# Optimization experiments

Hardware: AMD Instinct MI355X
Metric: run time of the kernel (lower is better)

## Reference

```python
import jax, jax.numpy as jnp
import numpy as np

OBS_DIM = 64; ACT_DIM = 18; INTER = 64; COMMAND = 32
UNITS = ACT_DIM + COMMAND + INTER  # 114; neuron order: [motor, command, inter]
Q_HIDDEN = max(32, UNITS)
B, T = 2048, 64
ODE_UNFOLDS = 6
EPS = 1e-8


def _build_wiring(seed=0):
    """NCP sparse wiring: sensory->inter, inter->command, command recurrent, command->motor."""
    rng = np.random.default_rng(seed)
    adj = np.zeros((UNITS, UNITS), np.float32)   # [pre, post]
    sens = np.zeros((OBS_DIM, UNITS), np.float32)
    motor = np.arange(ACT_DIM)
    cmd = np.arange(ACT_DIM, ACT_DIM + COMMAND)
    inter = np.arange(ACT_DIM + COMMAND, UNITS)
    for s in range(OBS_DIM):
        for d in rng.choice(inter, size=8, replace=False):
            sens[s, d] = rng.choice([-1.0, 1.0])
    for i in inter:
        for d in rng.choice(cmd, size=8, replace=False):
            adj[i, d] = rng.choice([-1.0, 1.0])
    for _ in range(32):
        adj[rng.choice(cmd), rng.choice(cmd)] = rng.choice([-1.0, 1.0])
    for m in motor:
        for s in rng.choice(cmd, size=8, replace=False):
            adj[s, m] = rng.choice([-1.0, 1.0])
    return adj, sens


def setup_inputs() -> dict:
    key = jax.random.key(0)
    ks = jax.random.split(key, 16)
    adj, sens = _build_wiring()
    u = lambda k, shape, lo, hi: jax.random.uniform(k, shape, jnp.float32, lo, hi)
    return {
        "obs": jax.random.normal(ks[0], (B, T, OBS_DIM), jnp.float32),
        "hidden": jnp.zeros((B, UNITS), jnp.float32),
        "input_w": jnp.ones((OBS_DIM,), jnp.float32),
        "input_b": jnp.zeros((OBS_DIM,), jnp.float32),
        "sensory_w": u(ks[1], (OBS_DIM, UNITS), 0.001, 1.0),
        "sensory_mu": u(ks[2], (OBS_DIM, UNITS), 0.3, 0.8),
        "sensory_sigma": u(ks[3], (OBS_DIM, UNITS), 3.0, 8.0),
        "sensory_erev": jnp.asarray(sens),
        "sensory_mask": jnp.asarray(np.abs(sens)),
        "w": u(ks[4], (UNITS, UNITS), 0.001, 1.0),
        "mu": u(ks[5], (UNITS, UNITS), 0.3, 0.8),
        "sigma": u(ks[6], (UNITS, UNITS), 3.0, 8.0),
        "erev": jnp.asarray(adj),
        "mask": jnp.asarray(np.abs(adj)),
        "gleak": u(ks[7], (UNITS,), 0.001, 1.0),
        "vleak": u(ks[8], (UNITS,), -0.2, 0.2),
        "cm": u(ks[9], (UNITS,), 0.4, 0.6),
        "q_w1": jax.random.normal(ks[10], (UNITS, Q_HIDDEN), jnp.float32) / np.sqrt(UNITS).astype(np.float32),
        "q_b1": jnp.zeros((Q_HIDDEN,), jnp.float32),
        "q_w2": jax.random.normal(ks[11], (Q_HIDDEN, ACT_DIM), jnp.float32) / np.sqrt(Q_HIDDEN).astype(np.float32),
        "q_b2": jnp.zeros((ACT_DIM,), jnp.float32),
    }


def _ltc_forward(obs, hidden, input_w, input_b, sensory_w, sensory_mu, sensory_sigma,
                 sensory_erev, sensory_mask, w, mu, sigma, erev, mask, gleak, vleak, cm):
    sw = sensory_w * sensory_mask          # sparse sensory synapses (S, U)
    ww = w * mask                          # sparse recurrent synapses (U, U)
    cm_t = cm * ODE_UNFOLDS                # cm / (elapsed_time / ode_unfolds), elapsed_time = 1.0

    @jax.checkpoint
    def step(h, x):
        xi = x * input_w + input_b                                                    # (B, S) affine input map
        s_act = sw * jax.nn.sigmoid((xi[:, :, None] - sensory_mu) * sensory_sigma)    # (B, S, U)
        w_num_s = jnp.sum(s_act * sensory_erev, axis=1)                               # (B, U)
        w_den_s = jnp.sum(s_act, axis=1)                                              # (B, U)

        def unfold(v, _):
            act = ww * jax.nn.sigmoid((v[:, :, None] - mu) * sigma)                   # (B, U, U)
            num = cm_t * v + gleak * vleak + jnp.sum(act * erev, axis=1) + w_num_s
            den = cm_t + gleak + jnp.sum(act, axis=1) + w_den_s
            return num / (den + EPS), None

        v, _ = jax.lax.scan(unfold, h, None, length=ODE_UNFOLDS)
        return v, None

    h, _ = jax.lax.scan(step, hidden, jnp.swapaxes(obs, 0, 1))  # scan over time
    return h


def reference(obs, hidden, input_w, input_b, sensory_w, sensory_mu, sensory_sigma,
              sensory_erev, sensory_mask, w, mu, sigma, erev, mask, gleak, vleak, cm,
              q_w1, q_b1, q_w2, q_b2):
    h = _ltc_forward(obs, hidden, input_w, input_b, sensory_w, sensory_mu, sensory_sigma,
                     sensory_erev, sensory_mask, w, mu, sigma, erev, mask, gleak, vleak, cm)
    q = jax.nn.relu(h @ q_w1 + q_b1) @ q_w2 + q_b2  # Q-head over full hidden state
    return q, h
```

## Files before the change

kernel.cpp:

```cpp
#include <hip/hip_runtime.h>

#define UNITS   114
#define SDIM    64
#define ACT     18
#define TSTEPS  64

#define CR 13
#define CS 9
#define ER_CAP 704
#define MSTRIDE 24

#define LOG2E 1.4426950408889634f
#define EPS   1e-8f

__device__ __forceinline__ float bperm(int addr, float v) {
  return __int_as_float(__builtin_amdgcn_ds_bpermute(addr, __float_as_int(v)));
}
__device__ __forceinline__ float dperm(int addr, float v) {
  return __int_as_float(__builtin_amdgcn_ds_permute(addr, __float_as_int(v)));
}
__device__ __forceinline__ float sigm(float msl, float nsgl, float x) {
  return __builtin_amdgcn_rcpf(1.f + __builtin_amdgcn_exp2f(fmaf(x, nsgl, msl)));
}
__device__ __forceinline__ void wsync() {
  __builtin_amdgcn_fence(__ATOMIC_ACQ_REL, "wavefront");
  __builtin_amdgcn_wave_barrier();
}
__device__ __forceinline__ int canonLane(int u) { return (u >= 64) ? (u - 64) : u; }

__device__ __forceinline__ int kthSetBit(unsigned long long m, int k) {
  int pos = 0;
#pragma unroll
  for (int ww = 32; ww >= 1; ww >>= 1) {
    const unsigned long long lowMask = ((1ull << ww) - 1ull);
    const int c = __popcll(m & lowMask);
    if (k >= c) { k -= c; m >>= ww; pos += ww; }
  }
  return pos;
}

__global__ __launch_bounds__(64) void build_all(
    const float* __restrict__ w,  const float* __restrict__ mu,
    const float* __restrict__ sigma, const float* __restrict__ erev,
    const float* __restrict__ mask,
    const float* __restrict__ sw, const float* __restrict__ smu,
    const float* __restrict__ ssg, const float* __restrict__ serev,
    const float* __restrict__ smask,
    float4* __restrict__ recP4, float2* __restrict__ recP2, int* __restrict__ recAd,
    float4* __restrict__ senP4, float2* __restrict__ senP2, int* __restrict__ senAd,
    int* __restrict__ meta)
{
  const int l = threadIdx.x;
  __shared__ short ePre[ER_CAP], ePIdx[ER_CAP];
  __shared__ int deg[64], off[65];
  __shared__ int pLane[64], pF0[64], pRole[64];
  __shared__ int contIdx[64], contOwn[64], splitRole[64], split2[64], ownP[128];
  __shared__ int rcv[64];

  contIdx[l] = 0; contOwn[l] = 0; splitRole[l] = -1; split2[l] = 0;
  ownP[2*l] = -1; ownP[2*l+1] = -1;
  pLane[l] = 0; pF0[l] = 0; pRole[l] = 0;

  if (blockIdx.x == 0) {
    int d = 0;
    if (l < 50) for (int i = 18; i < UNITS; ++i) d += (mask[i*UNITS + l] != 0.f) ? 1 : 0;
    deg[l] = (l < 50) ? d : 0;
    __syncthreads();
    if (l == 0) { int a = 0; for (int j = 0; j < 64; ++j) { off[j] = a; a += deg[j]; } off[64] = a; }
    __syncthreads();
    if (l < 50) {
      int o = off[l];
      for (int i = 18; i < UNITS; ++i)
        if (mask[i*UNITS + l] != 0.f) { ePre[o] = (short)i; ePIdx[o] = (short)l; ++o; }
    }
    if (l == 0) {
      int lam = 0, f = 0, pc = 0;
      for (int p = 0; p < 50; ++p) {
        const int dd = deg[p];
        if (pc == 2 || f == CR || dd > 3*CR - f) { ++lam; f = 0; pc = 0; }
        if (lam > 63) lam = 63;
        pLane[p] = lam; pF0[p] = f; pRole[p] = pc;
        ownP[2*lam + pc] = p;
        const int owner = lam, role = pc; ++pc;
        const int take = dd < (CR - f) ? dd : (CR - f);
        f += take; int rem = dd - take;
        if (rem > 0) {
          splitRole[owner] = role; split2[owner] = (rem > CR) ? 1 : 0;
          ++lam; if (lam > 63) lam = 63; contIdx[lam] = 1; contOwn[lam] = owner; pc = 1;
          const int t2 = rem < CR ? rem : CR; f = t2; rem -= t2;
          if (rem > 0) { ++lam; if (lam > 63) lam = 63; contIdx[lam] = 2; contOwn[lam] = owner; pc = 1; f = rem; }
        }
      }
    }
    __syncthreads();
    int dA = (contIdx[l] == 1) ? contOwn[l] : -1;
    int dB = (contIdx[l] == 2) ? contOwn[l] : -1;
    rcv[l] = 0; __syncthreads();
    if (dA >= 0) rcv[dA] = 1;
    __syncthreads();
    {
      const unsigned long long recvM = __ballot(rcv[l] != 0);
      const unsigned long long dumm  = __ballot(dA < 0);
      if (dA < 0) dA = kthSetBit(~recvM, __popcll(dumm & ((1ull << l) - 1ull)));
    }
    __syncthreads();
    rcv[l] = 0; __syncthreads();
    if (dB >= 0) rcv[dB] = 1;
    __syncthreads();
    {
      const unsigned long long recvM = __ballot(rcv[l] != 0);
      const unsigned long long dumm  = __ballot(dB < 0);
      if (dB < 0) dB = kthSetBit(~recvM, __popcll(dumm & ((1ull << l) - 1ull)));
    }
    {
      int* M = meta + l * MSTRIDE;
      M[0] = dA * 4; M[1] = dB * 4;
      const float s1A = (splitRole[l] == 0) ? 1.f : 0.f, s1B = (splitRole[l] == 1) ? 1.f : 0.f;
      M[2] = __float_as_int(s1A); M[3] = __float_as_int(s1B);
      const float s2 = split2[l] ? 1.f : 0.f;
      M[4] = __float_as_int(s1A * s2); M[5] = __float_as_int(s1B * s2);
      const int uA = ownP[2*l], uB = ownP[2*l+1];
      M[6] = ((uA >= 0) ? uA : 128 + l) * 4;
      M[7] = ((uB >= 0) ? uB : 192 + l) * 4;
      M[8] = (uA >= 0) ? uA : 0;
      M[9] = (uB >= 0) ? uB : 0;
    }
    for (int t = l; t < CR*64; t += 64) {
      recP4[t] = make_float4(0.f,0.f,0.f,0.f); recP2[t] = make_float2(0.f,0.f); recAd[t] = 0;
    }
    __syncthreads();
    {
      const int E = off[64];
      for (int e = l; e < E; e += 64) {
        const int pre = ePre[e], pj = ePIdx[e];
        const int r  = e - off[pj];
        const int dd = deg[pj], f0 = pF0[pj], role0 = pRole[pj];
        const int take = dd < (CR - f0) ? dd : (CR - f0);
        int lane = pLane[pj], slot, role;
        if (r < take)            { slot = f0 + r;        role = role0; }
        else if (r < take + CR)  { lane += 1; slot = r - take;      role = 0; }
        else                     { lane += 2; slot = r - take - CR; role = 0; }
        if (lane > 63) lane = 63;
        const int idx = pre * UNITS + pj;
        const float sg = sigma[idx];
        const float nsgl = -sg * LOG2E, msl = mu[idx] * sg * LOG2E;
        const float wd = w[idx], wn = wd * erev[idx];
        const int tt = slot * 64 + lane;
        recP4[tt] = make_float4(nsgl, msl, role ? 0.f : wn, role ? 0.f : wd);
        recP2[tt] = role ? make_float2(wn, wd) : make_float2(0.f, 0.f);
        recAd[tt] = pre * 4;
      }
    }
  } else {
    int d = 0;
    { const int col = 50 + l; for (int i = 0; i < SDIM; ++i) d += (smask[i*UNITS + col] != 0.f) ? 1 : 0; }
    deg[l] = d;
    __syncthreads();
    if (l == 0) { int a = 0; for (int j = 0; j < 64; ++j) { off[j] = a; a += deg[j]; } off[64] = a; }
    __syncthreads();
    {
      int o = off[l]; const int col = 50 + l;
      for (int i = 0; i < SDIM; ++i)
        if (smask[i*UNITS + col] != 0.f) { ePre[o] = (short)i; ePIdx[o] = (short)l; ++o; }
    }
    if (l == 0) {
      int lam = 0, f = 0, pc = 0;
      for (int p = 0; p < 64; ++p) {
        const int dd = deg[p];
        if (pc == 2 || f == CS || dd > 3*CS - f) { ++lam; f = 0; pc = 0; }
        if (lam > 63) lam = 63;
        pLane[p] = lam; pF0[p] = f; pRole[p] = pc;
        ownP[2*lam + pc] = p;
        const int owner = lam, role = pc; ++pc;
        const int take = dd < (CS - f) ? dd : (CS - f);
        f += take; int rem = dd - take;
        if (rem > 0) {
          splitRole[owner] = role; split2[owner] = (rem > CS) ? 1 : 0;
          ++lam; if (lam > 63) lam = 63; contIdx[lam] = 1; contOwn[lam] = owner; pc = 1;
          const int t2 = rem < CS ? rem : CS; f = t2; rem -= t2;
          if (rem > 0) { ++lam; if (lam > 63) lam = 63; contIdx[lam] = 2; contOwn[lam] = owner; pc = 1; f = rem; }
        }
      }
    }
    __syncthreads();
    int dA = (contIdx[l] == 1) ? contOwn[l] : -1;
    int dB = (contIdx[l] == 2) ? contOwn[l] : -1;
    rcv[l] = 0; __syncthreads();
    if (dA >= 0) rcv[dA] = 1;
    __syncthreads();
    {
      const unsigned long long recvM = __ballot(rcv[l] != 0);
      const unsigned long long dumm  = __ballot(dA < 0);
      if (dA < 0) dA = kthSetBit(~recvM, __popcll(dumm & ((1ull << l) - 1ull)));
    }
    __syncthreads();
    rcv[l] = 0; __syncthreads();
    if (dB >= 0) rcv[dB] = 1;
    __syncthreads();
    {
      const unsigned long long recvM = __ballot(rcv[l] != 0);
      const unsigned long long dumm  = __ballot(dB < 0);
      if (dB < 0) dB = kthSetBit(~recvM, __popcll(dumm & ((1ull << l) - 1ull)));
    }
    __syncthreads();
    int rA = (ownP[2*l]   >= 0) ? canonLane(50 + ownP[2*l])   : -1;
    int rB = (ownP[2*l+1] >= 0) ? canonLane(50 + ownP[2*l+1]) : -1;
    rcv[l] = 0; __syncthreads();
    if (rA >= 0) rcv[rA] = 1;
    __syncthreads();
    const int isRcvA = rcv[l];
    {
      const unsigned long long recvM = __ballot(isRcvA != 0);
      const unsigned long long dumm  = __ballot(rA < 0);
      if (rA < 0) rA = kthSetBit(~recvM, __popcll(dumm & ((1ull << l) - 1ull)));
    }
    __syncthreads();
    rcv[l] = 0; __syncthreads();
    if (rB >= 0) rcv[rB] = 1;
    __syncthreads();
    {
      const unsigned long long recvM = __ballot(rcv[l] != 0);
      const unsigned long long dumm  = __ballot(rB < 0);
      if (rB < 0) rB = kthSetBit(~recvM, __popcll(dumm & ((1ull << l) - 1ull)));
    }
    {
      int* M = meta + l * MSTRIDE;
      M[10] = dA * 4; M[11] = dB * 4;
      const float s1A = (splitRole[l] == 0) ? 1.f : 0.f, s1B = (splitRole[l] == 1) ? 1.f : 0.f;
      M[12] = __float_as_int(s1A); M[13] = __float_as_int(s1B);
      const float s2 = split2[l] ? 1.f : 0.f;
      M[14] = __float_as_int(s1A * s2); M[15] = __float_as_int(s1B * s2);
      M[16] = rA * 4; M[17] = rB * 4;
      M[18] = __float_as_int(isRcvA ? 1.f : 0.f);
      M[19] = __float_as_int(isRcvA ? 0.f : 1.f);
      const int pA = ownP[2*l], pB = ownP[2*l+1];
      M[20] = (pA >= 0) ? 50 + pA : 0;
      M[21] = (pB >= 0) ? 50 + pB : 0;
    }
    for (int t = l; t < CS*64; t += 64) {
      senP4[t] = make_float4(0.f,0.f,0.f,0.f); senP2[t] = make_float2(0.f,0.f); senAd[t] = 0;
    }
    __syncthreads();
    {
      const int E = off[64];
      for (int e = l; e < E; e += 64) {
        const int pre = ePre[e], pj = ePIdx[e];
        const int r  = e - off[pj];
        const int dd = deg[pj], f0 = pF0[pj], role0 = pRole[pj];
        const int take = dd < (CS - f0) ? dd : (CS - f0);
        int lane = pLane[pj], slot, role;
        if (r < take)            { slot = f0 + r;        role = role0; }
        else if (r < take + CS)  { lane += 1; slot = r - take;      role = 0; }
        else                     { lane += 2; slot = r - take - CS; role = 0; }
        if (lane > 63) lane = 63;
        const int col = 50 + pj;
        const int idx = pre * UNITS + col;
        const float sg = ssg[idx];
        const float nsgl = -sg * LOG2E, msl = smu[idx] * sg * LOG2E;
        const float wd = sw[idx], wn = wd * serev[idx];
        const int tt = slot * 64 + lane;
        senP4[tt] = make_float4(nsgl, msl, role ? 0.f : wn, role ? 0.f : wd);
        senP2[tt] = role ? make_float2(wn, wd) : make_float2(0.f, 0.f);
        senAd[tt] = pre * 4;
      }
    }
  }
}

__global__ __launch_bounds__(64, 2) void ltc_run(
    const float* __restrict__ obs,     const float* __restrict__ hidden,
    const float* __restrict__ input_w, const float* __restrict__ input_b,
    const float* __restrict__ gleak,   const float* __restrict__ vleak,
    const float* __restrict__ cm,
    const float* __restrict__ q_w1, const float* __restrict__ q_b1,
    const float* __restrict__ q_w2, const float* __restrict__ q_b2,
    const float4* __restrict__ recP4, const float2* __restrict__ recP2,
    const int* __restrict__ recAd,
    const float4* __restrict__ senP4, const float2* __restrict__ senP2,
    const int* __restrict__ senAd,
    const int* __restrict__ meta, float* __restrict__ out, int B)
{
  const int l = threadIdx.x, b = blockIdx.x;
  __shared__ float mirror[256];
  char* mbase = (char*)mirror;

  float4 rp4[CR]; float2 rp2[CR]; int rad[CR];
#pragma unroll
  for (int s = 0; s < CR; ++s) { rp4[s] = recP4[s*64+l]; rp2[s] = recP2[s*64+l]; rad[s] = recAd[s*64+l]; }
  float4 sp4[CS]; float2 sp2[CS]; int sad[CS];
#pragma unroll
  for (int s = 0; s < CS; ++s) { sp4[s] = senP4[s*64+l]; sp2[s] = senP2[s*64+l]; sad[s] = senAd[s*64+l]; }

  const int* M = meta + l * MSTRIDE;
  const int   rPush1 = M[0], rPush2 = M[1];
  const float rS1A = __int_as_float(M[2]), rS1B = __int_as_float(M[3]);
  const float rS2A = __int_as_float(M[4]), rS2B = __int_as_float(M[5]);
  const int   rWrA = M[6], rWrB = M[7], rUA = M[8], rUB = M[9];
  const int   sPush1 = M[10], sPush2 = M[11];
  const float sS1A = __int_as_float(M[12]), sS1B = __int_as_float(M[13]);
  const float sS2A = __int_as_float(M[14]), sS2B = __int_as_float(M[15]);
  const int   sRtA = M[16], sRtB = M[17];
  const float sRndA = __int_as_float(M[18]), sRndB = __int_as_float(M[19]);
  const int   sUA = M[20], sUB = M[21];

  const float cmA  = cm[rUA]*6.f, glvA  = gleak[rUA]*vleak[rUA], cgA  = cm[rUA]*6.f + gleak[rUA] + EPS;
  const float cmB  = cm[rUB]*6.f, glvB  = gleak[rUB]*vleak[rUB], cgB  = cm[rUB]*6.f + gleak[rUB] + EPS;
  const float cmSA = cm[sUA]*6.f, glvSA = gleak[sUA]*vleak[sUA], cgSA = cm[sUA]*6.f + gleak[sUA] + EPS;
  const float cmSB = cm[sUB]*6.f, glvSB = gleak[sUB]*vleak[sUB], cgSB = cm[sUB]*6.f + gleak[sUB] + EPS;

  const int  iUnit = (l < 50) ? 64 + l : l;
  const int  iWr   = iUnit * 4;
  float vIn = hidden[(size_t)b*UNITS + iUnit];
  float vPA = hidden[(size_t)b*UNITS + rUA];
  float vPB = hidden[(size_t)b*UNITS + rUB];

  mirror[l] = hidden[(size_t)b*UNITS + l];
  if (l < 50) mirror[64 + l] = hidden[(size_t)b*UNITS + 64 + l];

  const float iw = input_w[l], ibv = input_b[l];
  const float* ob = obs + (size_t)b*(TSTEPS*SDIM) + l;
  float xr = ob[0];

  for (int t = 0; t < TSTEPS; ++t) {
    const float xi = xr * iw + ibv;
    if (t + 1 < TSTEPS) xr = ob[(t + 1) * SDIM];

    float snA=0.f, sdA=0.f, snB=0.f, sdB=0.f;
#pragma unroll
    for (int s = 0; s < CS; ++s) {
      const float sg = sigm(sp4[s].y, sp4[s].x, bperm(sad[s], xi));
      snA = fmaf(sp4[s].z, sg, snA); sdA = fmaf(sp4[s].w, sg, sdA);
      snB = fmaf(sp2[s].x, sg, snB); sdB = fmaf(sp2[s].y, sg, sdB);
    }
    { const float rn = dperm(sPush1, snA), rd = dperm(sPush1, sdA);
      snA = fmaf(sS1A, rn, snA); sdA = fmaf(sS1A, rd, sdA);
      snB = fmaf(sS1B, rn, snB); sdB = fmaf(sS1B, rd, sdB); }
    { const float rn = dperm(sPush2, snA), rd = dperm(sPush2, sdA);
      snA = fmaf(sS2A, rn, snA); sdA = fmaf(sS2A, rd, sdA);
      snB = fmaf(sS2B, rn, snB); sdB = fmaf(sS2B, rd, sdB); }
    const float rdA_ = __builtin_amdgcn_rcpf(cgSA + sdA);
    const float aA_ = cmSA * rdA_, bA_ = (glvSA + snA) * rdA_;
    const float rdB_ = __builtin_amdgcn_rcpf(cgSB + sdB);
    const float aB_ = cmSB * rdB_, bB_ = (glvSB + snB) * rdB_;
    const float ra1 = dperm(sRtA, aA_), rb1 = dperm(sRtA, bA_);
    const float ra2 = dperm(sRtB, aB_), rb2 = dperm(sRtB, bB_);
    const float aI = sRndA * ra1 + sRndB * ra2;
    const float bI = sRndA * rb1 + sRndB * rb2;

#pragma unroll 1
    for (int u = 0; u < 6; ++u) {
      wsync();
      float nA=0.f, dA=0.f, nB=0.f, dB=0.f;
#pragma unroll
      for (int s = 0; s < CR; ++s) {
        const float pv = *(const float*)(mbase + rad[s]);
        const float sg = sigm(rp4[s].y, rp4[s].x, pv);
        nA = fmaf(rp4[s].z, sg, nA); dA = fmaf(rp4[s].w, sg, dA);
        nB = fmaf(rp2[s].x, sg, nB); dB = fmaf(rp2[s].y, sg, dB);
      }
      { const float rn = dperm(rPush1, nA), rd = dperm(rPush1, dA);
        nA = fmaf(rS1A, rn, nA); dA = fmaf(rS1A, rd, dA);
        nB = fmaf(rS1B, rn, nB); dB = fmaf(rS1B, rd, dB); }
      { const float rn = dperm(rPush2, nA), rd = dperm(rPush2, dA);
        nA = fmaf(rS2A, rn, nA); dA = fmaf(rS2A, rd, dA);
        nB = fmaf(rS2B, rn, nB); dB = fmaf(rS2B, rd, dB); }
      vPA = (fmaf(cmA, vPA, glvA) + nA) * __builtin_amdgcn_rcpf(cgA + dA);
      vPB = (fmaf(cmB, vPB, glvB) + nB) * __builtin_amdgcn_rcpf(cgB + dB);
      vIn = fmaf(aI, vIn, bI);
      wsync();
      *(float*)(mbase + rWrA) = vPA;
      *(float*)(mbase + rWrB) = vPB;
      *(float*)(mbase + iWr)  = vIn;
    }
  }
  wsync();

  float* __restrict__ outH = out + (size_t)B * ACT;
  outH[(size_t)b*UNITS + l] = mirror[l];
  if (l < 50) outH[(size_t)b*UNITS + 64 + l] = mirror[64 + l];

  const int j2 = (l < 50) ? 64 + l : l;
  float h1 = q_b1[l], h2 = q_b1[j2];
  for (int i = 0; i < UNITS; ++i) {
    const float hv = mirror[i];
    h1 = fmaf(hv, q_w1[i*UNITS + l],  h1);
    h2 = fmaf(hv, q_w1[i*UNITS + j2], h2);
  }
  h1 = fmaxf(h1, 0.f); h2 = fmaxf(h2, 0.f);
  wsync();
  mirror[l] = h1;
  if (l < 50) mirror[64 + l] = h2;
  wsync();
  if (l < ACT) {
    float q = q_b2[l];
    for (int i = 0; i < UNITS; ++i) q = fmaf(mirror[i], q_w2[i*ACT + l], q);
    out[(size_t)b*ACT + l] = q;
  }
}

extern "C" void kernel_launch(void* const* d_in, const int* in_sizes, int n_in,
                              void* d_out, int out_size, void* d_ws, size_t ws_size,
                              hipStream_t stream)
{
  const float* obs           = (const float*)d_in[0];
  const float* hidden        = (const float*)d_in[1];
  const float* input_w       = (const float*)d_in[2];
  const float* input_b       = (const float*)d_in[3];
  const float* sensory_w     = (const float*)d_in[4];
  const float* sensory_mu    = (const float*)d_in[5];
  const float* sensory_sigma = (const float*)d_in[6];
  const float* sensory_erev  = (const float*)d_in[7];
  const float* sensory_mask  = (const float*)d_in[8];
  const float* w             = (const float*)d_in[9];
  const float* mu            = (const float*)d_in[10];
  const float* sigma         = (const float*)d_in[11];
  const float* erev          = (const float*)d_in[12];
  const float* mask          = (const float*)d_in[13];
  const float* gleak         = (const float*)d_in[14];
  const float* vleak         = (const float*)d_in[15];
  const float* cm            = (const float*)d_in[16];
  const float* q_w1          = (const float*)d_in[17];
  const float* q_b1          = (const float*)d_in[18];
  const float* q_w2          = (const float*)d_in[19];
  const float* q_b2          = (const float*)d_in[20];

  char* ws = (char*)d_ws;
  float4* recP4 = (float4*)(ws);
  float2* recP2 = (float2*)(ws + 13312);
  int*    recAd = (int*)   (ws + 19968);
  float4* senP4 = (float4*)(ws + 23296);
  float2* senP2 = (float2*)(ws + 32512);
  int*    senAd = (int*)   (ws + 37120);
  int*    meta  = (int*)   (ws + 39424);

  build_all<<<2, 64, 0, stream>>>(
      w, mu, sigma, erev, mask,
      sensory_w, sensory_mu, sensory_sigma, sensory_erev, sensory_mask,
      recP4, recP2, recAd, senP4, senP2, senAd, meta);

  const int B = in_sizes[0] / (TSTEPS * SDIM);
  ltc_run<<<B, 64, 0, stream>>>(
      obs, hidden, input_w, input_b, gleak, vleak, cm,
      q_w1, q_b1, q_w2, q_b2,
      recP4, recP2, recAd, senP4, senP2, senAd, meta,
      (float*)d_out, B);
}
```

Measured before the change: 404.3 us.

## Precompute sensory terms in separate parallel kernel and batch sigmoid reciprocals

Moves the sensory-synapse evaluation out of the sequential time loop into a separate fully parallel kernel (one wave per batch-time pair) that writes per-step (a,b) coefficients to workspace. The recurrent kernel then streams these values with a one-step prefetch. It also shares one reciprocal across groups of four sigmoids and uses packed v2f FMAs for the accumulations. The trade-off is extra global memory traffic and an extra launch. The sigmoid input is clamped to keep the shared reciprocal from overflowing, and the path depends on the workspace being large enough, with a fallback to the old kernel if it is not.

```diff
diff --git a/kernel.cpp b/kernel.cpp
--- a/kernel.cpp
+++ b/kernel.cpp
@@ -13,14 +13,15 @@
 #define LOG2E 1.4426950408889634f
 #define EPS   1e-8f
 
+typedef float v2f __attribute__((ext_vector_type(2)));
+__device__ __forceinline__ v2f fma2(v2f a, v2f b, v2f c) {
+  return __builtin_elementwise_fma(a, b, c);
+}
 __device__ __forceinline__ float bperm(int addr, float v) {
   return __int_as_float(__builtin_amdgcn_ds_bpermute(addr, __float_as_int(v)));
 }
 __device__ __forceinline__ float dperm(int addr, float v) {
   return __int_as_float(__builtin_amdgcn_ds_permute(addr, __float_as_int(v)));
-}
-__device__ __forceinline__ float sigm(float msl, float nsgl, float x) {
-  return __builtin_amdgcn_rcpf(1.f + __builtin_amdgcn_exp2f(fmaf(x, nsgl, msl)));
 }
 __device__ __forceinline__ void wsync() {
   __builtin_amdgcn_fence(__ATOMIC_ACQ_REL, "wavefront");
@@ -98,20 +99,14 @@
     rcv[l] = 0; __syncthreads();
     if (dA >= 0) rcv[dA] = 1;
     __syncthreads();
-    {
-      const unsigned long long recvM = __ballot(rcv[l] != 0);
-      const unsigned long long dumm  = __ballot(dA < 0);
-      if (dA < 0) dA = kthSetBit(~recvM, __popcll(dumm & ((1ull << l) - 1ull)));
-    }
+    { const unsigned long long rM = __ballot(rcv[l] != 0), dM = __ballot(dA < 0);
+      if (dA < 0) dA = kthSetBit(~rM, __popcll(dM & ((1ull << l) - 1ull))); }
     __syncthreads();
     rcv[l] = 0; __syncthreads();
     if (dB >= 0) rcv[dB] = 1;
     __syncthreads();
-    {
-      const unsigned long long recvM = __ballot(rcv[l] != 0);
-      const unsigned long long dumm  = __ballot(dB < 0);
-      if (dB < 0) dB = kthSetBit(~recvM, __popcll(dumm & ((1ull << l) - 1ull)));
-    }
+    { const unsigned long long rM = __ballot(rcv[l] != 0), dM = __ballot(dB < 0);
+      if (dB < 0) dB = kthSetBit(~rM, __popcll(dM & ((1ull << l) - 1ull))); }
     {
       int* M = meta + l * MSTRIDE;
       M[0] = dA * 4; M[1] = dB * 4;
@@ -188,20 +183,14 @@
     rcv[l] = 0; __syncthreads();
     if (dA >= 0) rcv[dA] = 1;
     __syncthreads();
-    {
-      const unsigned long long recvM = __ballot(rcv[l] != 0);
-      const unsigned long long dumm  = __ballot(dA < 0);
-      if (dA < 0) dA = kthSetBit(~recvM, __popcll(dumm & ((1ull << l) - 1ull)));
-    }
+    { const unsigned long long rM = __ballot(rcv[l] != 0), dM = __ballot(dA < 0);
+      if (dA < 0) dA = kthSetBit(~rM, __popcll(dM & ((1ull << l) - 1ull))); }
     __syncthreads();
     rcv[l] = 0; __syncthreads();
     if (dB >= 0) rcv[dB] = 1;
     __syncthreads();
-    {
-      const unsigned long long recvM = __ballot(rcv[l] != 0);
-      const unsigned long long dumm  = __ballot(dB < 0);
-      if (dB < 0) dB = kthSetBit(~recvM, __popcll(dumm & ((1ull << l) - 1ull)));
-    }
+    { const unsigned long long rM = __ballot(rcv[l] != 0), dM = __ballot(dB < 0);
+      if (dB < 0) dB = kthSetBit(~rM, __popcll(dM & ((1ull << l) - 1ull))); }
     __syncthreads();
     int rA = (ownP[2*l]   >= 0) ? canonLane(50 + ownP[2*l])   : -1;
     int rB = (ownP[2*l+1] >= 0) ? canonLane(50 + ownP[2*l+1]) : -1;
@@ -209,20 +198,14 @@
     if (rA >= 0) rcv[rA] = 1;
     __syncthreads();
     const int isRcvA = rcv[l];
-    {
-      const unsigned long long recvM = __ballot(isRcvA != 0);
-      const unsigned long long dumm  = __ballot(rA < 0);
-      if (rA < 0) rA = kthSetBit(~recvM, __popcll(dumm & ((1ull << l) - 1ull)));
-    }
+    { const unsigned long long rM = __ballot(isRcvA != 0), dM = __ballot(rA < 0);
+      if (rA < 0) rA = kthSetBit(~rM, __popcll(dM & ((1ull << l) - 1ull))); }
     __syncthreads();
     rcv[l] = 0; __syncthreads();
     if (rB >= 0) rcv[rB] = 1;
     __syncthreads();
-    {
-      const unsigned long long recvM = __ballot(rcv[l] != 0);
-      const unsigned long long dumm  = __ballot(rB < 0);
-      if (rB < 0) rB = kthSetBit(~recvM, __popcll(dumm & ((1ull << l) - 1ull)));
-    }
+    { const unsigned long long rM = __ballot(rcv[l] != 0), dM = __ballot(rB < 0);
+      if (rB < 0) rB = kthSetBit(~rM, __popcll(dM & ((1ull << l) - 1ull))); }
     {
       int* M = meta + l * MSTRIDE;
       M[10] = dA * 4; M[11] = dB * 4;
@@ -267,6 +250,91 @@
   }
 }
 
+__device__ __forceinline__ float2 sensory_eval(
+    const float xi,
+    const float* sNS, const float* sMS, const v2f* sWA, const v2f* sWB,
+    const int* sad,
+    int sPush1, int sPush2, v2f gS1A, v2f gS1B, v2f gS2A, v2f gS2B,
+    int sRtA, int sRtB, float sRndA, float sRndB,
+    float cmSA, float glvSA, float cgSA, float cmSB, float glvSB, float cgSB)
+{
+  float u[CS];
+#pragma unroll
+  for (int s = 0; s < CS; ++s) {
+    float z = fmaf(bperm(sad[s], xi), sNS[s], sMS[s]);
+    z = fminf(z, 30.f);
+    u[s] = 1.f + __builtin_amdgcn_exp2f(z);
+  }
+  float sg[CS];
+#pragma unroll
+  for (int q = 0; q < 2; ++q) {
+    const int s0 = 4*q;
+    const float p01 = u[s0]*u[s0+1], p23 = u[s0+2]*u[s0+3];
+    const float r = __builtin_amdgcn_rcpf(p01*p23);
+    const float t23 = p23*r, t01 = p01*r;
+    sg[s0]   = u[s0+1]*t23; sg[s0+1] = u[s0]*t23;
+    sg[s0+2] = u[s0+3]*t01; sg[s0+3] = u[s0+2]*t01;
+  }
+  sg[8] = __builtin_amdgcn_rcpf(u[8]);
+  v2f cA = {0.f, 0.f}, cB = {0.f, 0.f};
+#pragma unroll
+  for (int s = 0; s < CS; ++s) {
+    const v2f s2 = {sg[s], sg[s]};
+    cA = fma2(sWA[s], s2, cA);
+    cB = fma2(sWB[s], s2, cB);
+  }
+  const v2f m1 = {dperm(sPush1, cA.x), dperm(sPush1, cA.y)};
+  const v2f m2 = {dperm(sPush2, cA.x), dperm(sPush2, cA.y)};
+  v2f tA = fma2(gS1A, m1, cA); tA = fma2(gS2A, m2, tA);
+  v2f tB = fma2(gS1B, m1, cB); tB = fma2(gS2B, m2, tB);
+  const float rdA = __builtin_amdgcn_rcpf(cgSA + tA.y);
+  const float aA = cmSA * rdA, bA = (glvSA + tA.x) * rdA;
+  const float rdB = __builtin_amdgcn_rcpf(cgSB + tB.y);
+  const float aB = cmSB * rdB, bB = (glvSB + tB.x) * rdB;
+  const float ra1 = dperm(sRtA, aA), rb1 = dperm(sRtA, bA);
+  const float ra2 = dperm(sRtB, aB), rb2 = dperm(sRtB, bB);
+  return make_float2(sRndA*ra1 + sRndB*ra2, sRndA*rb1 + sRndB*rb2);
+}
+
+__global__ __launch_bounds__(256) void sens_pre(
+    const float* __restrict__ obs, const float* __restrict__ input_w,
+    const float* __restrict__ input_b,
+    const float* __restrict__ gleak, const float* __restrict__ vleak,
+    const float* __restrict__ cm,
+    const float4* __restrict__ senP4, const float2* __restrict__ senP2,
+    const int* __restrict__ senAd, const int* __restrict__ meta,
+    float2* __restrict__ sAB, int B)
+{
+  const int l = threadIdx.x & 63;
+  const int wv = blockIdx.x * 4 + (threadIdx.x >> 6);
+  const int b = wv >> 6, t = wv & 63;
+  if (b >= B) return;
+
+  float sNS[CS], sMS[CS]; v2f sWA[CS], sWB[CS]; int sad[CS];
+#pragma unroll
+  for (int s = 0; s < CS; ++s) {
+    const float4 p4 = senP4[s*64 + l]; const float2 p2 = senP2[s*64 + l];
+    sNS[s] = p4.x; sMS[s] = p4.y; sWA[s] = (v2f){p4.z, p4.w};
+    sWB[s] = (v2f){p2.x, p2.y}; sad[s] = senAd[s*64 + l];
+  }
+  const int* M = meta + l * MSTRIDE;
+  const int   sPush1 = M[10], sPush2 = M[11];
+  const float sS1A = __int_as_float(M[12]), sS1B = __int_as_float(M[13]);
+  const float sS2A = __int_as_float(M[14]), sS2B = __int_as_float(M[15]);
+  const int   sRtA = M[16], sRtB = M[17];
+  const float sRndA = __int_as_float(M[18]), sRndB = __int_as_float(M[19]);
+  const int   sUA = M[20], sUB = M[21];
+  const float cmSA = cm[sUA]*6.f, glvSA = gleak[sUA]*vleak[sUA], cgSA = cm[sUA]*6.f + gleak[sUA] + EPS;
+  const float cmSB = cm[sUB]*6.f, glvSB = gleak[sUB]*vleak[sUB], cgSB = cm[sUB]*6.f + gleak[sUB] + EPS;
+
+  const float xi = obs[((size_t)b*TSTEPS + t)*SDIM + l] * input_w[l] + input_b[l];
+  const float2 ab = sensory_eval(xi, sNS, sMS, sWA, sWB, sad,
+      sPush1, sPush2, (v2f){sS1A,sS1A}, (v2f){sS1B,sS1B}, (v2f){sS2A,sS2A}, (v2f){sS2B,sS2B},
+      sRtA, sRtB, sRndA, sRndB, cmSA, glvSA, cgSA, cmSB, glvSB, cgSB);
+  sAB[((size_t)b*TSTEPS + t)*64 + l] = ab;
+}
+
+template <int SENS>
 __global__ __launch_bounds__(64, 2) void ltc_run(
     const float* __restrict__ obs,     const float* __restrict__ hidden,
     const float* __restrict__ input_w, const float* __restrict__ input_b,
@@ -278,35 +346,51 @@
     const int* __restrict__ recAd,
     const float4* __restrict__ senP4, const float2* __restrict__ senP2,
     const int* __restrict__ senAd,
-    const int* __restrict__ meta, float* __restrict__ out, int B)
+    const int* __restrict__ meta, const float2* __restrict__ sAB,
+    float* __restrict__ out, int B)
 {
   const int l = threadIdx.x, b = blockIdx.x;
   __shared__ float mirror[256];
   char* mbase = (char*)mirror;
 
-  float4 rp4[CR]; float2 rp2[CR]; int rad[CR];
-#pragma unroll
-  for (int s = 0; s < CR; ++s) { rp4[s] = recP4[s*64+l]; rp2[s] = recP2[s*64+l]; rad[s] = recAd[s*64+l]; }
-  float4 sp4[CS]; float2 sp2[CS]; int sad[CS];
-#pragma unroll
-  for (int s = 0; s < CS; ++s) { sp4[s] = senP4[s*64+l]; sp2[s] = senP2[s*64+l]; sad[s] = senAd[s*64+l]; }
-
+  float rNS[CR], rMS[CR]; v2f rWA[CR], rWB[CR]; int rad[CR];
+#pragma unroll
+  for (int s = 0; s < CR; ++s) {
+    const float4 p4 = recP4[s*64 + l]; const float2 p2 = recP2[s*64 + l];
+    rNS[s] = p4.x; rMS[s] = p4.y; rWA[s] = (v2f){p4.z, p4.w};
+    rWB[s] = (v2f){p2.x, p2.y}; rad[s] = recAd[s*64 + l];
+  }
   const int* M = meta + l * MSTRIDE;
   const int   rPush1 = M[0], rPush2 = M[1];
-  const float rS1A = __int_as_float(M[2]), rS1B = __int_as_float(M[3]);
-  const float rS2A = __int_as_float(M[4]), rS2B = __int_as_float(M[5]);
+  const v2f gR1A = {__int_as_float(M[2]), __int_as_float(M[2])};
+  const v2f gR1B = {__int_as_float(M[3]), __int_as_float(M[3])};
+  const v2f gR2A = {__int_as_float(M[4]), __int_as_float(M[4])};
+  const v2f gR2B = {__int_as_float(M[5]), __int_as_float(M[5])};
   const int   rWrA = M[6], rWrB = M[7], rUA = M[8], rUB = M[9];
-  const int   sPush1 = M[10], sPush2 = M[11];
-  const float sS1A = __int_as_float(M[12]), sS1B = __int_as_float(M[13]);
-  const float sS2A = __int_as_float(M[14]), sS2B = __int_as_float(M[15]);
-  const int   sRtA = M[16], sRtB = M[17];
-  const float sRndA = __int_as_float(M[18]), sRndB = __int_as_float(M[19]);
-  const int   sUA = M[20], sUB = M[21];
-
-  const float cmA  = cm[rUA]*6.f, glvA  = gleak[rUA]*vleak[rUA], cgA  = cm[rUA]*6.f + gleak[rUA] + EPS;
-  const float cmB  = cm[rUB]*6.f, glvB  = gleak[rUB]*vleak[rUB], cgB  = cm[rUB]*6.f + gleak[rUB] + EPS;
-  const float cmSA = cm[sUA]*6.f, glvSA = gleak[sUA]*vleak[sUA], cgSA = cm[sUA]*6.f + gleak[sUA] + EPS;
-  const float cmSB = cm[sUB]*6.f, glvSB = gleak[sUB]*vleak[sUB], cgSB = cm[sUB]*6.f + gleak[sUB] + EPS;
+
+  float sNS[CS], sMS[CS]; v2f sWA[CS], sWB[CS]; int sad[CS];
+  int sPush1=0, sPush2=0, sRtA=0, sRtB=0;
+  float sS1A=0, sS1B=0, sS2A=0, sS2B=0, sRndA=0, sRndB=0;
+  float cmSA=0, glvSA=0, cgSA=0, cmSB=0, glvSB=0, cgSB=0;
+  if (SENS == 0) {
+#pragma unroll
+    for (int s = 0; s < CS; ++s) {
+      const float4 p4 = senP4[s*64 + l]; const float2 p2 = senP2[s*64 + l];
+      sNS[s] = p4.x; sMS[s] = p4.y; sWA[s] = (v2f){p4.z, p4.w};
+      sWB[s] = (v2f){p2.x, p2.y}; sad[s] = senAd[s*64 + l];
+    }
+    sPush1 = M[10]; sPush2 = M[11];
+    sS1A = __int_as_float(M[12]); sS1B = __int_as_float(M[13]);
+    sS2A = __int_as_float(M[14]); sS2B = __int_as_float(M[15]);
+    sRtA = M[16]; sRtB = M[17];
+    sRndA = __int_as_float(M[18]); sRndB = __int_as_float(M[19]);
+    const int sUA = M[20], sUB = M[21];
+    cmSA = cm[sUA]*6.f; glvSA = gleak[sUA]*vleak[sUA]; cgSA = cm[sUA]*6.f + gleak[sUA] + EPS;
+    cmSB = cm[sUB]*6.f; glvSB = gleak[sUB]*vleak[sUB]; cgSB = cm[sUB]*6.f + gleak[sUB] + EPS;
+  }
+
+  const float cmA = cm[rUA]*6.f, glvA = gleak[rUA]*vleak[rUA], cgA = cm[rUA]*6.f + gleak[rUA] + EPS;
+  const float cmB = cm[rUB]*6.f, glvB = gleak[rUB]*vleak[rUB], cgB = cm[rUB]*6.f + gleak[rUB] + EPS;
 
   const int  iUnit = (l < 50) ? 64 + l : l;
   const int  iWr   = iUnit * 4;
@@ -317,61 +401,73 @@
   mirror[l] = hidden[(size_t)b*UNITS + l];
   if (l < 50) mirror[64 + l] = hidden[(size_t)b*UNITS + 64 + l];
 
-  const float iw = input_w[l], ibv = input_b[l];
+  const float iw = (SENS == 0) ? input_w[l] : 0.f;
+  const float ibv = (SENS == 0) ? input_b[l] : 0.f;
   const float* ob = obs + (size_t)b*(TSTEPS*SDIM) + l;
-  float xr = ob[0];
+  float xr = (SENS == 0) ? ob[0] : 0.f;
+
+  const float2* sBase = sAB + (size_t)b*TSTEPS*64 + l;
+  float2 abC, abN;
+  if (SENS == 1) abC = sBase[0];
 
   for (int t = 0; t < TSTEPS; ++t) {
-    const float xi = xr * iw + ibv;
-    if (t + 1 < TSTEPS) xr = ob[(t + 1) * SDIM];
-
-    float snA=0.f, sdA=0.f, snB=0.f, sdB=0.f;
-#pragma unroll
-    for (int s = 0; s < CS; ++s) {
-      const float sg = sigm(sp4[s].y, sp4[s].x, bperm(sad[s], xi));
-      snA = fmaf(sp4[s].z, sg, snA); sdA = fmaf(sp4[s].w, sg, sdA);
-      snB = fmaf(sp2[s].x, sg, snB); sdB = fmaf(sp2[s].y, sg, sdB);
-    }
-    { const float rn = dperm(sPush1, snA), rd = dperm(sPush1, sdA);
-      snA = fmaf(sS1A, rn, snA); sdA = fmaf(sS1A, rd, sdA);
-      snB = fmaf(sS1B, rn, snB); sdB = fmaf(sS1B, rd, sdB); }
-    { const float rn = dperm(sPush2, snA), rd = dperm(sPush2, sdA);
-      snA = fmaf(sS2A, rn, snA); sdA = fmaf(sS2A, rd, sdA);
-      snB = fmaf(sS2B, rn, snB); sdB = fmaf(sS2B, rd, sdB); }
-    const float rdA_ = __builtin_amdgcn_rcpf(cgSA + sdA);
-    const float aA_ = cmSA * rdA_, bA_ = (glvSA + snA) * rdA_;
-    const float rdB_ = __builtin_amdgcn_rcpf(cgSB + sdB);
-    const float aB_ = cmSB * rdB_, bB_ = (glvSB + snB) * rdB_;
-    const float ra1 = dperm(sRtA, aA_), rb1 = dperm(sRtA, bA_);
-    const float ra2 = dperm(sRtB, aB_), rb2 = dperm(sRtB, bB_);
-    const float aI = sRndA * ra1 + sRndB * ra2;
-    const float bI = sRndA * rb1 + sRndB * rb2;
+    float aI, bI;
+    if (SENS == 1) {
+      aI = abC.x; bI = abC.y;
+      if (t + 1 < TSTEPS) abN = sBase[(t + 1) * 64];
+    } else {
+      const float xi = xr * iw + ibv;
+      if (t + 1 < TSTEPS) xr = ob[(t + 1) * SDIM];
+      const float2 ab = sensory_eval(xi, sNS, sMS, sWA, sWB, sad,
+          sPush1, sPush2, (v2f){sS1A,sS1A}, (v2f){sS1B,sS1B},
+          (v2f){sS2A,sS2A}, (v2f){sS2B,sS2B},
+          sRtA, sRtB, sRndA, sRndB, cmSA, glvSA, cgSA, cmSB, glvSB, cgSB);
+      aI = ab.x; bI = ab.y;
+    }
 
 #pragma unroll 1
-    for (int u = 0; u < 6; ++u) {
+    for (int u_ = 0; u_ < 6; ++u_) {
       wsync();
-      float nA=0.f, dA=0.f, nB=0.f, dB=0.f;
+      float u[CR];
 #pragma unroll
       for (int s = 0; s < CR; ++s) {
         const float pv = *(const float*)(mbase + rad[s]);
-        const float sg = sigm(rp4[s].y, rp4[s].x, pv);
-        nA = fmaf(rp4[s].z, sg, nA); dA = fmaf(rp4[s].w, sg, dA);
-        nB = fmaf(rp2[s].x, sg, nB); dB = fmaf(rp2[s].y, sg, dB);
-      }
-      { const float rn = dperm(rPush1, nA), rd = dperm(rPush1, dA);
-        nA = fmaf(rS1A, rn, nA); dA = fmaf(rS1A, rd, dA);
-        nB = fmaf(rS1B, rn, nB); dB = fmaf(rS1B, rd, dB); }
-      { const float rn = dperm(rPush2, nA), rd = dperm(rPush2, dA);
-        nA = fmaf(rS2A, rn, nA); dA = fmaf(rS2A, rd, dA);
-        nB = fmaf(rS2B, rn, nB); dB = fmaf(rS2B, rd, dB); }
-      vPA = (fmaf(cmA, vPA, glvA) + nA) * __builtin_amdgcn_rcpf(cgA + dA);
-      vPB = (fmaf(cmB, vPB, glvB) + nB) * __builtin_amdgcn_rcpf(cgB + dB);
+        float z = fmaf(pv, rNS[s], rMS[s]);
+        z = fminf(z, 30.f);
+        u[s] = 1.f + __builtin_amdgcn_exp2f(z);
+      }
+      float sg[CR];
+#pragma unroll
+      for (int q = 0; q < 3; ++q) {
+        const int s0 = 4*q;
+        const float p01 = u[s0]*u[s0+1], p23 = u[s0+2]*u[s0+3];
+        const float r = __builtin_amdgcn_rcpf(p01*p23);
+        const float t23 = p23*r, t01 = p01*r;
+        sg[s0]   = u[s0+1]*t23; sg[s0+1] = u[s0]*t23;
+        sg[s0+2] = u[s0+3]*t01; sg[s0+3] = u[s0+2]*t01;
+      }
+      sg[12] = __builtin_amdgcn_rcpf(u[12]);
+      v2f aA = {0.f, 0.f}, aB = {0.f, 0.f};
+#pragma unroll
+      for (int s = 0; s < CR; ++s) {
+        const v2f s2 = {sg[s], sg[s]};
+        aA = fma2(rWA[s], s2, aA);
+        aB = fma2(rWB[s], s2, aB);
+      }
+      const v2f m1 = {dperm(rPush1, aA.x), dperm(rPush1, aA.y)};
+      const v2f m2 = {dperm(rPush2, aA.x), dperm(rPush2, aA.y)};
+      v2f tA = fma2(gR1A, m1, aA); tA = fma2(gR2A, m2, tA);
+      v2f tB = fma2(gR1B, m1, aB); tB = fma2(gR2B, m2, tB);
+
+      vPA = (fmaf(cmA, vPA, glvA) + tA.x) * __builtin_amdgcn_rcpf(cgA + tA.y);
+      vPB = (fmaf(cmB, vPB, glvB) + tB.x) * __builtin_amdgcn_rcpf(cgB + tB.y);
       vIn = fmaf(aI, vIn, bI);
       wsync();
       *(float*)(mbase + rWrA) = vPA;
       *(float*)(mbase + rWrB) = vPB;
       *(float*)(mbase + iWr)  = vIn;
     }
+    if (SENS == 1) abC = abN;
   }
   wsync();
 
@@ -432,16 +528,31 @@
   float2* senP2 = (float2*)(ws + 32512);
   int*    senAd = (int*)   (ws + 37120);
   int*    meta  = (int*)   (ws + 39424);
+  const size_t sABoff = 65536;
+  float2* sAB   = (float2*)(ws + sABoff);
+
+  const int B = in_sizes[0] / (TSTEPS * SDIM);
+  const size_t need = sABoff + (size_t)B * TSTEPS * 64 * sizeof(float2);
 
   build_all<<<2, 64, 0, stream>>>(
       w, mu, sigma, erev, mask,
       sensory_w, sensory_mu, sensory_sigma, sensory_erev, sensory_mask,
       recP4, recP2, recAd, senP4, senP2, senAd, meta);
 
-  const int B = in_sizes[0] / (TSTEPS * SDIM);
-  ltc_run<<<B, 64, 0, stream>>>(
-      obs, hidden, input_w, input_b, gleak, vleak, cm,
-      q_w1, q_b1, q_w2, q_b2,
-      recP4, recP2, recAd, senP4, senP2, senAd, meta,
-      (float*)d_out, B);
-}
+  if (ws_size >= need) {
+    sens_pre<<<B * 16, 256, 0, stream>>>(
+        obs, input_w, input_b, gleak, vleak, cm,
+        senP4, senP2, senAd, meta, sAB, B);
+    ltc_run<1><<<B, 64, 0, stream>>>(
+        obs, hidden, input_w, input_b, gleak, vleak, cm,
+        q_w1, q_b1, q_w2, q_b2,
+        recP4, recP2, recAd, senP4, senP2, senAd, meta, sAB,
+        (float*)d_out, B);
+  } else {
+    ltc_run<0><<<B, 64, 0, stream>>>(
+        obs, hidden, input_w, input_b, gleak, vleak, cm,
+        q_w1, q_b1, q_w2, q_b2,
+        recP4, recP2, recAd, senP4, senP2, senAd, meta, sAB,
+        (float*)d_out, B);
+  }
+}
```

After: 568.4 us. 40.6% more time.
